# Performance work log

Hardware: AMD Instinct MI355X
Metric: run time of the kernel (lower is better)

## Reference

```python
import jax, jax.numpy as jnp
import numpy as np

TEMPERATURE = 0.5
B, D = 4096, 256


def setup_inputs() -> dict:
    key = jax.random.key(0)
    k1, k2 = jax.random.split(key)
    z_i = jax.random.normal(k1, (B, D), dtype=jnp.float32)
    z_j = jax.random.normal(k2, (B, D), dtype=jnp.float32)
    return {"z_i": z_i, "z_j": z_j}


def reference(z_i, z_j):
    batch = z_i.shape[0]
    n = 2 * batch
    z = jnp.concatenate([z_i, z_j], axis=0)                      # [2B, D]
    z = z / jnp.linalg.norm(z, axis=1, keepdims=True)            # L2-normalize rows
    # cosine_similarity of unit vectors == dot product -> single GEMM
    sim = jnp.einsum('id,jd->ij', z, z) / TEMPERATURE            # [2B, 2B]
    mask = jnp.eye(n, dtype=bool)
    sim = jnp.where(mask, -jnp.inf, sim)                         # mask self-similarity
    positives = jnp.concatenate(
        [jnp.diagonal(sim, offset=batch), jnp.diagonal(sim, offset=-batch)], axis=0
    )                                                            # [2B]
    loss = -positives + jax.nn.logsumexp(sim, axis=1)            # [2B]
    return loss.mean()
```

## Files before the change

kernel.cpp:

```cpp
#include <hip/hip_runtime.h>
#include <hip/hip_bf16.h>
#include <stdint.h>
#include <stddef.h>


#define B_ROWS 4096
#define D_DIM  256
#define N_ROWS 8192
#define BM 128
#define BN 128

typedef __bf16 bf16;
typedef bf16  bf16x8  __attribute__((ext_vector_type(8)));
typedef bf16  bf16x4  __attribute__((ext_vector_type(4)));
typedef float floatx4 __attribute__((ext_vector_type(4)));

__global__ __launch_bounds__(256) void normalize_kernel(
    const float* __restrict__ z_i, const float* __restrict__ z_j,
    bf16* __restrict__ zn, float* __restrict__ sumexp) {
  const int wave = threadIdx.x >> 6;
  const int lane = threadIdx.x & 63;
  const int row  = blockIdx.x * 4 + wave;
  const float* src = (row < B_ROWS) ? (z_i + (size_t)row * D_DIM)
                                    : (z_j + (size_t)(row - B_ROWS) * D_DIM);
  float4 v = ((const float4*)src)[lane];
  float ss = v.x * v.x + v.y * v.y + v.z * v.z + v.w * v.w;
  #pragma unroll
  for (int m = 1; m < 64; m <<= 1) ss += __shfl_xor(ss, m);
  const float rn = rsqrtf(ss) * 1.6986436f;
  bf16x4 o;
  o[0] = (bf16)(v.x * rn);
  o[1] = (bf16)(v.y * rn);
  o[2] = (bf16)(v.z * rn);
  o[3] = (bf16)(v.w * rn);
  ((bf16x4*)(zn + (size_t)row * D_DIM))[lane] = o;
  if (lane == 0) sumexp[row] = 0.f;
}

__global__ __launch_bounds__(512, 2) void simexp_kernel(
    const bf16* __restrict__ zn, float* __restrict__ sumexp,
    float* __restrict__ pos) {
  __shared__ __align__(16) bf16 Bs[2][BN * D_DIM];

  const int tid   = threadIdx.x;
  const int wave  = tid >> 6;
  const int lane  = tid & 63;
  const int lcol  = lane & 15;
  const int lquad = lane >> 4;
  const int wr = (wave >> 1) * 32;
  const int wc = (wave & 1) * 64;
  const int ri = blockIdx.x >> 2;
  const int cj = blockIdx.x & 3;
  const int row_base = ri * BM;
  const bool has_tail = (ri < 32 && cj >= 2);

  auto ct_of = [&](int t) { return (ri + 8 * cj + t) & 63; };

  auto stageB = [&](int buf, const bf16* src, int it0, int it1) {
    for (int it = it0; it < it1; ++it) {
      const int s   = it * 512 + tid;
      const int n   = s >> 5;
      const int kcs = s & 31;
      const int kc  = (kcs & 24) | ((kcs & 7) ^ (n & 7));
      __builtin_amdgcn_global_load_lds(
          (const __attribute__((address_space(1))) unsigned int*)
              (src + (size_t)n * D_DIM + kc * 8),
          (__attribute__((address_space(3))) unsigned int*)&Bs[buf][s * 8],
          16, 0, 0);
    }
  };

  stageB(0, zn + (size_t)row_base * D_DIM, 0, 8);
  stageB(1, zn + (size_t)ct_of(0) * BM * D_DIM, 0, 8);
  __syncthreads();

  floatx4 af[2][8];
  #pragma unroll
  for (int ti = 0; ti < 2; ++ti) {
    const int n = wr + ti * 16 + lcol;
    #pragma unroll
    for (int kq = 0; kq < 8; ++kq) {
      const int kc  = kq * 4 + lquad;
      const int kcs = (kc & 24) | ((kc & 7) ^ (n & 7));
      af[ti][kq] = *(const floatx4*)(&Bs[0][(n * 32 + kcs) * 8]);
    }
  }
  __syncthreads();

  float rowsum[2][4];
  #pragma unroll
  for (int ti = 0; ti < 2; ++ti)
    #pragma unroll
    for (int r = 0; r < 4; ++r) rowsum[ti][r] = 0.f;

#define MFMA_(A, B_, C) __builtin_amdgcn_mfma_f32_16x16x32_bf16( \
    __builtin_bit_cast(bf16x8, A), B_, C, 0, 0, 0)

#define QPHASE(ACC, Q)                                                    \
  {                                                                       \
    bf16x8 bfr[8];                                                        \
    const int n = wc + (Q) * 16 + lcol;                                   \
    _Pragma("unroll")                                                     \
    for (int kq = 0; kq < 8; ++kq) {                                      \
      const int kc  = kq * 4 + lquad;                                     \
      const int kcs = (kc & 24) | ((kc & 7) ^ (n & 7));                   \
      bfr[kq] = *(const bf16x8*)(bbase + n * D_DIM + kcs * 8);            \
    }                                                                     \
    ACC[0] = floatx4{0.f, 0.f, 0.f, 0.f};                                 \
    ACC[1] = floatx4{0.f, 0.f, 0.f, 0.f};                                 \
    _Pragma("unroll")                                                     \
    for (int kq = 0; kq < 8; ++kq) {                                      \
      ACC[0] = MFMA_(af[0][kq], bfr[kq], ACC[0]);                         \
      ACC[1] = MFMA_(af[1][kq], bfr[kq], ACC[1]);                         \
    }                                                                     \
  }

#define SLICE(ACC, Q, CB, DG)                                             \
  {                                                                       \
    float cs = 0.f;                                                       \
    _Pragma("unroll")                                                     \
    for (int ti = 0; ti < 2; ++ti) {                                      \
      _Pragma("unroll")                                                   \
      for (int r = 0; r < 4; ++r) {                                       \
        const float v = ACC[ti][r];                                       \
        float e = __builtin_amdgcn_exp2f(v);                              \
        if (DG) {                                                         \
          const int rg = row_base + wr + ti * 16 + lquad * 4 + r;         \
          const int cg = (CB) + wc + (Q) * 16 + lcol;                     \
          if (cg == rg) e = 0.f;                \
        }                                                                 \
        rowsum[ti][r] += e;                                               \
        cs += e;                                                          \
      }                                                                   \
    }                                                                     \
    cs += __shfl_xor(cs, 16);                                             \
    cs += __shfl_xor(cs, 32);                                             \
    if (!(DG) && lquad == 0)                                              \
      atomicAdd(&sumexp[(CB) + wc + (Q) * 16 + lcol], cs);                \
  }

  floatx4 a3[2];
  int  pcol3  = 0;
  bool pdiag3 = false;

  #pragma unroll 1
  for (int t = 0; t < 8; ++t) {
    const bf16* bbase = &Bs[(t + 1) & 1][0];
    const int sb = t & 1;
    if (t < 7) {
      stageB(sb, zn + (size_t)ct_of(t + 1) * BM * D_DIM, 0, 8);
    } else if (has_tail) {
      stageB(sb, zn + (size_t)((ri + 32) * BM + (cj - 2) * 64) * D_DIM, 0, 4);
    }
    const int  colb = ct_of(t) * BM;
    const bool diag = (cj == 0 && t == 0);

    floatx4 a0[2], a1[2], a2[2];
    QPHASE(a0, 0)
    if (t > 0) SLICE(a3, 3, pcol3, pdiag3)
    QPHASE(a1, 1)
    SLICE(a0, 0, colb, diag)
    QPHASE(a2, 2)
    SLICE(a1, 1, colb, diag)
    QPHASE(a3, 3)
    SLICE(a2, 2, colb, diag)
    pcol3 = colb;
    pdiag3 = diag;
    __syncthreads();
  }
  SLICE(a3, 3, pcol3, pdiag3)

  if (has_tail && wc == 0) {
    const int colb = (ri + 32) * BM + (cj - 2) * 64;
    const bf16* bbase = &Bs[1][0];
    floatx4 ta[2];
    #pragma unroll
    for (int Q = 0; Q < 4; ++Q) {
      QPHASE(ta, Q)
      float cs = 0.f;
      #pragma unroll
      for (int ti = 0; ti < 2; ++ti) {
        #pragma unroll
        for (int r = 0; r < 4; ++r) {
          const float v = ta[ti][r];
          const float e = __builtin_amdgcn_exp2f(v);
          const int rg = row_base + wr + ti * 16 + lquad * 4 + r;
          const int cg = colb + Q * 16 + lcol;
          if (cg == rg + B_ROWS) {
            const float p = v * 0.6931471805599453f;
            pos[rg] = p;
            pos[cg] = p;
          }
          rowsum[ti][r] += e;
          cs += e;
        }
      }
      cs += __shfl_xor(cs, 16);
      cs += __shfl_xor(cs, 32);
      if (lquad == 0) atomicAdd(&sumexp[colb + Q * 16 + lcol], cs);
    }
  }
#undef SLICE
#undef QPHASE
#undef MFMA_

  #pragma unroll
  for (int ti = 0; ti < 2; ++ti) {
    #pragma unroll
    for (int r = 0; r < 4; ++r) {
      float s2 = rowsum[ti][r];
      s2 += __shfl_xor(s2, 1);
      s2 += __shfl_xor(s2, 2);
      s2 += __shfl_xor(s2, 4);
      s2 += __shfl_xor(s2, 8);
      if (lcol == 0) {
        const int grow = row_base + wr + ti * 16 + lquad * 4 + r;
        atomicAdd(&sumexp[grow], s2);
      }
    }
  }
}

__global__ __launch_bounds__(1024) void reduce_kernel(
    const float* __restrict__ sumexp, const float* __restrict__ pos,
    float* __restrict__ out) {
  __shared__ float ws[16];
  const int tid = threadIdx.x;
  float s = 0.f;
  const float ln2 = 0.6931471805599453f;
  for (int k = tid; k < N_ROWS; k += 1024)
    s += __builtin_amdgcn_logf(sumexp[k]) * ln2 - pos[k];
  #pragma unroll
  for (int m = 1; m < 64; m <<= 1) s += __shfl_xor(s, m);
  const int wave = tid >> 6, lane = tid & 63;
  if (lane == 0) ws[wave] = s;
  __syncthreads();
  if (wave == 0) {
    float t = (lane < 16) ? ws[lane] : 0.f;
    #pragma unroll
    for (int m = 1; m < 16; m <<= 1) t += __shfl_xor(t, m);
    if (lane == 0) out[0] = t * (1.0f / N_ROWS);
  }
}

extern "C" void kernel_launch(void* const* d_in, const int* in_sizes, int n_in,
                              void* d_out, int out_size, void* d_ws,
                              size_t ws_size, hipStream_t stream) {
  const float* z_i = (const float*)d_in[0];
  const float* z_j = (const float*)d_in[1];
  float* out = (float*)d_out;

  bf16* zn = (bf16*)d_ws;
  float* sumexp = (float*)((char*)d_ws + (size_t)N_ROWS * D_DIM * sizeof(bf16));
  float* pos = sumexp + N_ROWS;

  normalize_kernel<<<N_ROWS / 4, 256, 0, stream>>>(z_i, z_j, zn, sumexp);
  simexp_kernel<<<256, 512, 0, stream>>>(zn, sumexp, pos);
  reduce_kernel<<<1, 1024, 0, stream>>>(sumexp, pos, out);
}
```

Baseline: 92.08 us.

## Stage B tiles in K-halves with finer pipelining and LDS column-sum accumulation

Splits each B tile into two K-halves held in a 4-slot LDS ring. Loads of the next tile's halves overlap MFMA on the current halves, synchronised with explicit vmcnt waits and raw s_barrier instead of full __syncthreads. Column-sum partials now go to LDS atomics and are flushed to global once per block, which cuts global atomic traffic. MFMA sections also get s_setprio boosts. The cost is more LDS (two extra buffers' worth plus a colsum array) and fragile hand-tuned waitcnt logic.

```diff
diff --git a/kernel.cpp b/kernel.cpp
--- a/kernel.cpp
+++ b/kernel.cpp
@@ -8,7 +8,6 @@
 #define D_DIM  256
 #define N_ROWS 8192
 #define BM 128
-#define BN 128
 
 typedef __bf16 bf16;
 typedef bf16  bf16x8  __attribute__((ext_vector_type(8)));
@@ -40,7 +39,8 @@
 __global__ __launch_bounds__(512, 2) void simexp_kernel(
     const bf16* __restrict__ zn, float* __restrict__ sumexp,
     float* __restrict__ pos) {
-  __shared__ __align__(16) bf16 Bs[2][BN * D_DIM];
+  __shared__ __align__(16) bf16 Hs[4][128 * 128];
+  __shared__ float colsum_s[9 * 128];
 
   const int tid   = threadIdx.x;
   const int wave  = tid >> 6;
@@ -56,8 +56,23 @@
 
   auto ct_of = [&](int t) { return (ri + 8 * cj + t) & 63; };
 
-  auto stageB = [&](int buf, const bf16* src, int it0, int it1) {
-    for (int it = it0; it < it1; ++it) {
+  auto stage_half = [&](int buf, const bf16* src, int kh) {
+    #pragma unroll
+    for (int it = 0; it < 4; ++it) {
+      const int s   = it * 512 + tid;
+      const int n   = s >> 4;
+      const int lcs = s & 15;
+      const int lc  = (lcs & 8) | ((lcs & 7) ^ (n & 7));
+      __builtin_amdgcn_global_load_lds(
+          (const __attribute__((address_space(1))) unsigned int*)
+              (src + (size_t)n * D_DIM + kh * 128 + lc * 8),
+          (__attribute__((address_space(3))) unsigned int*)&Hs[buf][s * 8],
+          16, 0, 0);
+    }
+  };
+  auto stage_tail = [&](int buf, const bf16* src) {
+    #pragma unroll
+    for (int it = 0; it < 4; ++it) {
       const int s   = it * 512 + tid;
       const int n   = s >> 5;
       const int kcs = s & 31;
@@ -65,14 +80,22 @@
       __builtin_amdgcn_global_load_lds(
           (const __attribute__((address_space(1))) unsigned int*)
               (src + (size_t)n * D_DIM + kc * 8),
-          (__attribute__((address_space(3))) unsigned int*)&Bs[buf][s * 8],
+          (__attribute__((address_space(3))) unsigned int*)&Hs[buf][s * 8],
           16, 0, 0);
     }
   };
 
-  stageB(0, zn + (size_t)row_base * D_DIM, 0, 8);
-  stageB(1, zn + (size_t)ct_of(0) * BM * D_DIM, 0, 8);
-  __syncthreads();
+  const bf16* Abase  = zn + (size_t)row_base * D_DIM;
+  const bf16* B0base = zn + (size_t)ct_of(0) * BM * D_DIM;
+  stage_half(0, Abase, 0);
+  stage_half(1, Abase, 1);
+  stage_half(2, B0base, 0);
+  stage_half(3, B0base, 1);
+  #pragma unroll 1
+  for (int s = tid; s < 9 * 128; s += 512) colsum_s[s] = 0.f;
+  asm volatile("s_waitcnt vmcnt(8)" ::: "memory");
+  __builtin_amdgcn_sched_barrier(0);
+  __builtin_amdgcn_s_barrier();
 
   floatx4 af[2][8];
   #pragma unroll
@@ -80,12 +103,15 @@
     const int n = wr + ti * 16 + lcol;
     #pragma unroll
     for (int kq = 0; kq < 8; ++kq) {
-      const int kc  = kq * 4 + lquad;
-      const int kcs = (kc & 24) | ((kc & 7) ^ (n & 7));
-      af[ti][kq] = *(const floatx4*)(&Bs[0][(n * 32 + kcs) * 8]);
-    }
-  }
-  __syncthreads();
+      const int kql = kq & 3;
+      const int lc  = kql * 4 + lquad;
+      const int lcs = (lc & 8) | ((lc & 7) ^ (n & 7));
+      af[ti][kq] = *(const floatx4*)(&Hs[kq >> 2][n * 128 + lcs * 8]);
+    }
+  }
+  asm volatile("s_waitcnt lgkmcnt(0)" ::: "memory");
+  __builtin_amdgcn_sched_barrier(0);
+  __builtin_amdgcn_s_barrier();
 
   float rowsum[2][4];
   #pragma unroll
@@ -96,26 +122,35 @@
 #define MFMA_(A, B_, C) __builtin_amdgcn_mfma_f32_16x16x32_bf16( \
     __builtin_bit_cast(bf16x8, A), B_, C, 0, 0, 0)
 
-#define QPHASE(ACC, Q)                                                    \
+#define QPHASE(ACC, Q, KH, BB)                                            \
   {                                                                       \
-    bf16x8 bfr[8];                                                        \
     const int n = wc + (Q) * 16 + lcol;                                   \
-    _Pragma("unroll")                                                     \
-    for (int kq = 0; kq < 8; ++kq) {                                      \
-      const int kc  = kq * 4 + lquad;                                     \
-      const int kcs = (kc & 24) | ((kc & 7) ^ (n & 7));                   \
-      bfr[kq] = *(const bf16x8*)(bbase + n * D_DIM + kcs * 8);            \
-    }                                                                     \
-    ACC[0] = floatx4{0.f, 0.f, 0.f, 0.f};                                 \
-    ACC[1] = floatx4{0.f, 0.f, 0.f, 0.f};                                 \
-    _Pragma("unroll")                                                     \
-    for (int kq = 0; kq < 8; ++kq) {                                      \
-      ACC[0] = MFMA_(af[0][kq], bfr[kq], ACC[0]);                         \
-      ACC[1] = MFMA_(af[1][kq], bfr[kq], ACC[1]);                         \
-    }                                                                     \
-  }
-
-#define SLICE(ACC, Q, CB, DG)                                             \
+    bf16x8 b0, b1, b2, b3;                                                \
+    { const int lc = 0 * 4 + lquad;                                       \
+      b0 = *(const bf16x8*)((BB) + n * 128 +                              \
+           (((lc & 8) | ((lc & 7) ^ (n & 7))) * 8)); }                    \
+    { const int lc = 1 * 4 + lquad;                                       \
+      b1 = *(const bf16x8*)((BB) + n * 128 +                              \
+           (((lc & 8) | ((lc & 7) ^ (n & 7))) * 8)); }                    \
+    { const int lc = 2 * 4 + lquad;                                       \
+      b2 = *(const bf16x8*)((BB) + n * 128 +                              \
+           (((lc & 8) | ((lc & 7) ^ (n & 7))) * 8)); }                    \
+    { const int lc = 3 * 4 + lquad;                                       \
+      b3 = *(const bf16x8*)((BB) + n * 128 +                              \
+           (((lc & 8) | ((lc & 7) ^ (n & 7))) * 8)); }                    \
+    __builtin_amdgcn_s_setprio(1);                                        \
+    ACC[0] = MFMA_(af[0][(KH)*4 + 0], b0, ACC[0]);                        \
+    ACC[1] = MFMA_(af[1][(KH)*4 + 0], b0, ACC[1]);                        \
+    ACC[0] = MFMA_(af[0][(KH)*4 + 1], b1, ACC[0]);                        \
+    ACC[1] = MFMA_(af[1][(KH)*4 + 1], b1, ACC[1]);                        \
+    ACC[0] = MFMA_(af[0][(KH)*4 + 2], b2, ACC[0]);                        \
+    ACC[1] = MFMA_(af[1][(KH)*4 + 2], b2, ACC[1]);                        \
+    ACC[0] = MFMA_(af[0][(KH)*4 + 3], b3, ACC[0]);                        \
+    ACC[1] = MFMA_(af[1][(KH)*4 + 3], b3, ACC[1]);                        \
+    __builtin_amdgcn_s_setprio(0);                                        \
+  }
+
+#define SLICE(ACC, Q, SLOT, COLB, DG)                                     \
   {                                                                       \
     float cs = 0.f;                                                       \
     _Pragma("unroll")                                                     \
@@ -126,8 +161,8 @@
         float e = __builtin_amdgcn_exp2f(v);                              \
         if (DG) {                                                         \
           const int rg = row_base + wr + ti * 16 + lquad * 4 + r;         \
-          const int cg = (CB) + wc + (Q) * 16 + lcol;                     \
-          if (cg == rg) e = 0.f;                \
+          const int cg = (COLB) + wc + (Q) * 16 + lcol;                   \
+          if (cg == rg) e = 0.f;                                          \
         }                                                                 \
         rowsum[ti][r] += e;                                               \
         cs += e;                                                          \
@@ -136,73 +171,139 @@
     cs += __shfl_xor(cs, 16);                                             \
     cs += __shfl_xor(cs, 32);                                             \
     if (!(DG) && lquad == 0)                                              \
-      atomicAdd(&sumexp[(CB) + wc + (Q) * 16 + lcol], cs);                \
-  }
-
-  floatx4 a3[2];
-  int  pcol3  = 0;
+      atomicAdd(&colsum_s[(SLOT) + wc + (Q) * 16 + lcol], cs);            \
+  }
+
+  floatx4 acc0[2], acc1[2], acc2[2], acc3[2];
+  floatx4 car[2];
+  int  pslot3 = 0, pcolb3 = 0;
   bool pdiag3 = false;
 
   #pragma unroll 1
   for (int t = 0; t < 8; ++t) {
-    const bf16* bbase = &Bs[(t + 1) & 1][0];
-    const int sb = t & 1;
-    if (t < 7) {
-      stageB(sb, zn + (size_t)ct_of(t + 1) * BM * D_DIM, 0, 8);
-    } else if (has_tail) {
-      stageB(sb, zn + (size_t)((ri + 32) * BM + (cj - 2) * 64) * D_DIM, 0, 4);
-    }
     const int  colb = ct_of(t) * BM;
     const bool diag = (cj == 0 && t == 0);
 
-    floatx4 a0[2], a1[2], a2[2];
-    QPHASE(a0, 0)
-    if (t > 0) SLICE(a3, 3, pcol3, pdiag3)
-    QPHASE(a1, 1)
-    SLICE(a0, 0, colb, diag)
-    QPHASE(a2, 2)
-    SLICE(a1, 1, colb, diag)
-    QPHASE(a3, 3)
-    SLICE(a2, 2, colb, diag)
-    pcol3 = colb;
-    pdiag3 = diag;
-    __syncthreads();
-  }
-  SLICE(a3, 3, pcol3, pdiag3)
-
-  if (has_tail && wc == 0) {
-    const int colb = (ri + 32) * BM + (cj - 2) * 64;
-    const bf16* bbase = &Bs[1][0];
-    floatx4 ta[2];
-    #pragma unroll
-    for (int Q = 0; Q < 4; ++Q) {
-      QPHASE(ta, Q)
-      float cs = 0.f;
+    {
+      const int h = 2 * t;
+      if (t < 7) {
+        stage_half(h & 3, zn + (size_t)ct_of(t + 1) * BM * D_DIM, 0);
+        asm volatile("s_waitcnt vmcnt(8)" ::: "memory");
+      } else if (has_tail) {
+        stage_tail(h & 3,
+                   zn + (size_t)((ri + 32) * BM + (cj - 2) * 64) * D_DIM);
+        asm volatile("s_waitcnt vmcnt(8)" ::: "memory");
+      } else {
+        asm volatile("s_waitcnt vmcnt(4)" ::: "memory");
+      }
+      __builtin_amdgcn_sched_barrier(0);
+      __builtin_amdgcn_s_barrier();
+      const bf16* bb = &Hs[(h + 2) & 3][0];
       #pragma unroll
       for (int ti = 0; ti < 2; ++ti) {
+        acc0[ti] = floatx4{0.f, 0.f, 0.f, 0.f};
+        acc1[ti] = floatx4{0.f, 0.f, 0.f, 0.f};
+        acc2[ti] = floatx4{0.f, 0.f, 0.f, 0.f};
+        acc3[ti] = floatx4{0.f, 0.f, 0.f, 0.f};
+      }
+      QPHASE(acc0, 0, 0, bb)
+      QPHASE(acc1, 1, 0, bb)
+      QPHASE(acc2, 2, 0, bb)
+      QPHASE(acc3, 3, 0, bb)
+    }
+
+    {
+      const int h = 2 * t + 1;
+      if (t < 7) {
+        stage_half(h & 3, zn + (size_t)ct_of(t + 1) * BM * D_DIM, 1);
+        asm volatile("s_waitcnt vmcnt(8)" ::: "memory");
+      } else if (has_tail) {
+        asm volatile("s_waitcnt vmcnt(4)" ::: "memory");
+      } else {
+        asm volatile("s_waitcnt vmcnt(0)" ::: "memory");
+      }
+      __builtin_amdgcn_sched_barrier(0);
+      __builtin_amdgcn_s_barrier();
+      const bf16* bb = &Hs[(h + 2) & 3][0];
+      QPHASE(acc0, 0, 1, bb)
+      if (t > 0) SLICE(car, 3, pslot3, pcolb3, pdiag3)
+      QPHASE(acc1, 1, 1, bb)
+      SLICE(acc0, 0, t * 128, colb, diag)
+      QPHASE(acc2, 2, 1, bb)
+      SLICE(acc1, 1, t * 128, colb, diag)
+      QPHASE(acc3, 3, 1, bb)
+      SLICE(acc2, 2, t * 128, colb, diag)
+      car[0] = acc3[0];
+      car[1] = acc3[1];
+      pslot3 = t * 128;
+      pcolb3 = colb;
+      pdiag3 = diag;
+    }
+  }
+  SLICE(car, 3, pslot3, pcolb3, pdiag3)
+
+  if (has_tail) {
+    asm volatile("s_waitcnt vmcnt(0)" ::: "memory");
+    __builtin_amdgcn_sched_barrier(0);
+    __builtin_amdgcn_s_barrier();
+    if (wc == 0) {
+      const int colb = (ri + 32) * BM + (cj - 2) * 64;
+      const bf16* bb = &Hs[2][0];
+      #pragma unroll
+      for (int Q = 0; Q < 4; ++Q) {
+        const int n = Q * 16 + lcol;
+        floatx4 ta[2];
+        ta[0] = floatx4{0.f, 0.f, 0.f, 0.f};
+        ta[1] = floatx4{0.f, 0.f, 0.f, 0.f};
         #pragma unroll
-        for (int r = 0; r < 4; ++r) {
-          const float v = ta[ti][r];
-          const float e = __builtin_amdgcn_exp2f(v);
-          const int rg = row_base + wr + ti * 16 + lquad * 4 + r;
-          const int cg = colb + Q * 16 + lcol;
-          if (cg == rg + B_ROWS) {
-            const float p = v * 0.6931471805599453f;
-            pos[rg] = p;
-            pos[cg] = p;
+        for (int kq = 0; kq < 8; ++kq) {
+          const int kc  = kq * 4 + lquad;
+          const int kcs = (kc & 24) | ((kc & 7) ^ (n & 7));
+          const bf16x8 b = *(const bf16x8*)(bb + n * 256 + kcs * 8);
+          ta[0] = MFMA_(af[0][kq], b, ta[0]);
+          ta[1] = MFMA_(af[1][kq], b, ta[1]);
+        }
+        float cs = 0.f;
+        #pragma unroll
+        for (int ti = 0; ti < 2; ++ti) {
+          #pragma unroll
+          for (int r = 0; r < 4; ++r) {
+            const float v = ta[ti][r];
+            const float e = __builtin_amdgcn_exp2f(v);
+            const int rg = row_base + wr + ti * 16 + lquad * 4 + r;
+            const int cg = colb + Q * 16 + lcol;
+            if (cg == rg + B_ROWS) {
+              const float p = v * 0.6931471805599453f;
+              pos[rg] = p;
+              pos[cg] = p;
+            }
+            rowsum[ti][r] += e;
+            cs += e;
           }
-          rowsum[ti][r] += e;
-          cs += e;
         }
-      }
-      cs += __shfl_xor(cs, 16);
-      cs += __shfl_xor(cs, 32);
-      if (lquad == 0) atomicAdd(&sumexp[colb + Q * 16 + lcol], cs);
+        cs += __shfl_xor(cs, 16);
+        cs += __shfl_xor(cs, 32);
+        if (lquad == 0) atomicAdd(&colsum_s[8 * 128 + Q * 16 + lcol], cs);
+      }
     }
   }
 #undef SLICE
 #undef QPHASE
 #undef MFMA_
+
+  __syncthreads();
+
+  #pragma unroll 1
+  for (int s = tid; s < 9 * 128; s += 512) {
+    const int tile = s >> 7, col = s & 127;
+    const float v = colsum_s[s];
+    if (tile < 8) {
+      if (!(cj == 0 && tile == 0))
+        atomicAdd(&sumexp[ct_of(tile) * BM + col], v);
+    } else if (has_tail && col < 64) {
+      atomicAdd(&sumexp[(ri + 32) * BM + (cj - 2) * 64 + col], v);
+    }
+  }
 
   #pragma unroll
   for (int ti = 0; ti < 2; ++ti) {
```

Result: slower. 95.49 us (+3.7%).

## Reshape per-wave tile to 64x32 so each B fragment feeds four MFMAs

Applied to the files above, without the earlier changes.

Changes the 8-wave layout from 4x2 waves of 32x64 sub-tiles to 2x4 waves of 64x32 sub-tiles. Each wave now holds four A row-fragments in registers and loads half as many B fragments from LDS per tile, reusing each across four MFMAs. The software pipeline is restructured from four column phases to two, with a carried accumulator overlapping exp work of one phase with the next phase's MFMAs. The doubled A fragments and accumulators raise register pressure, and the launch bounds are relaxed to 1 min block with waves_per_eu(2) to give the compiler room.

```diff
diff --git a/kernel.cpp b/kernel.cpp
--- a/kernel.cpp
+++ b/kernel.cpp
@@ -8,7 +8,6 @@
 #define D_DIM  256
 #define N_ROWS 8192
 #define BM 128
-#define BN 128
 
 typedef __bf16 bf16;
 typedef bf16  bf16x8  __attribute__((ext_vector_type(8)));
@@ -37,18 +36,20 @@
   if (lane == 0) sumexp[row] = 0.f;
 }
 
-__global__ __launch_bounds__(512, 2) void simexp_kernel(
+__global__ __launch_bounds__(512, 1)
+__attribute__((amdgpu_waves_per_eu(2)))
+void simexp_kernel(
     const bf16* __restrict__ zn, float* __restrict__ sumexp,
     float* __restrict__ pos) {
-  __shared__ __align__(16) bf16 Bs[2][BN * D_DIM];
+  __shared__ __align__(16) bf16 Bs[2][BM * D_DIM];
 
   const int tid   = threadIdx.x;
   const int wave  = tid >> 6;
   const int lane  = tid & 63;
   const int lcol  = lane & 15;
   const int lquad = lane >> 4;
-  const int wr = (wave >> 1) * 32;
-  const int wc = (wave & 1) * 64;
+  const int wr = (wave >> 2) * 64;
+  const int wc = (wave & 3) * 32;
   const int ri = blockIdx.x >> 2;
   const int cj = blockIdx.x & 3;
   const int row_base = ri * BM;
@@ -74,9 +75,9 @@
   stageB(1, zn + (size_t)ct_of(0) * BM * D_DIM, 0, 8);
   __syncthreads();
 
-  floatx4 af[2][8];
-  #pragma unroll
-  for (int ti = 0; ti < 2; ++ti) {
+  floatx4 af[4][8];
+  #pragma unroll
+  for (int ti = 0; ti < 4; ++ti) {
     const int n = wr + ti * 16 + lcol;
     #pragma unroll
     for (int kq = 0; kq < 8; ++kq) {
@@ -87,46 +88,47 @@
   }
   __syncthreads();
 
-  float rowsum[2][4];
-  #pragma unroll
-  for (int ti = 0; ti < 2; ++ti)
+  float rowsum[4][4];
+  #pragma unroll
+  for (int ti = 0; ti < 4; ++ti)
     #pragma unroll
     for (int r = 0; r < 4; ++r) rowsum[ti][r] = 0.f;
 
 #define MFMA_(A, B_, C) __builtin_amdgcn_mfma_f32_16x16x32_bf16( \
     __builtin_bit_cast(bf16x8, A), B_, C, 0, 0, 0)
 
-#define QPHASE(ACC, Q)                                                    \
+#define PHASE_(ACC, NCOL, BB)                                             \
   {                                                                       \
+    const int n = (NCOL);                                                 \
     bf16x8 bfr[8];                                                        \
-    const int n = wc + (Q) * 16 + lcol;                                   \
     _Pragma("unroll")                                                     \
     for (int kq = 0; kq < 8; ++kq) {                                      \
       const int kc  = kq * 4 + lquad;                                     \
       const int kcs = (kc & 24) | ((kc & 7) ^ (n & 7));                   \
-      bfr[kq] = *(const bf16x8*)(bbase + n * D_DIM + kcs * 8);            \
+      bfr[kq] = *(const bf16x8*)((BB) + n * D_DIM + kcs * 8);             \
     }                                                                     \
-    ACC[0] = floatx4{0.f, 0.f, 0.f, 0.f};                                 \
-    ACC[1] = floatx4{0.f, 0.f, 0.f, 0.f};                                 \
+    _Pragma("unroll")                                                     \
+    for (int ti = 0; ti < 4; ++ti) ACC[ti] = floatx4{0.f, 0.f, 0.f, 0.f}; \
     _Pragma("unroll")                                                     \
     for (int kq = 0; kq < 8; ++kq) {                                      \
-      ACC[0] = MFMA_(af[0][kq], bfr[kq], ACC[0]);                         \
-      ACC[1] = MFMA_(af[1][kq], bfr[kq], ACC[1]);                         \
+      _Pragma("unroll")                                                   \
+      for (int ti = 0; ti < 4; ++ti)                                      \
+        ACC[ti] = MFMA_(af[ti][kq], bfr[kq], ACC[ti]);                    \
     }                                                                     \
   }
 
-#define SLICE(ACC, Q, CB, DG)                                             \
+#define SLICE(ACC, CGB, DG)                                               \
   {                                                                       \
     float cs = 0.f;                                                       \
     _Pragma("unroll")                                                     \
-    for (int ti = 0; ti < 2; ++ti) {                                      \
+    for (int ti = 0; ti < 4; ++ti) {                                      \
       _Pragma("unroll")                                                   \
       for (int r = 0; r < 4; ++r) {                                       \
         const float v = ACC[ti][r];                                       \
         float e = __builtin_amdgcn_exp2f(v);                              \
         if (DG) {                                                         \
           const int rg = row_base + wr + ti * 16 + lquad * 4 + r;         \
-          const int cg = (CB) + wc + (Q) * 16 + lcol;                     \
+          const int cg = (CGB) + lcol;                                    \
           if (cg == rg) e = 0.f;                \
         }                                                                 \
         rowsum[ti][r] += e;                                               \
@@ -135,13 +137,12 @@
     }                                                                     \
     cs += __shfl_xor(cs, 16);                                             \
     cs += __shfl_xor(cs, 32);                                             \
-    if (!(DG) && lquad == 0)                                              \
-      atomicAdd(&sumexp[(CB) + wc + (Q) * 16 + lcol], cs);                \
-  }
-
-  floatx4 a3[2];
-  int  pcol3  = 0;
-  bool pdiag3 = false;
+    if (!(DG) && lquad == 0) atomicAdd(&sumexp[(CGB) + lcol], cs);        \
+  }
+
+  floatx4 accA[4], accB[4], carry[4];
+  int  pcgb  = 0;
+  bool pdiag = false;
 
   #pragma unroll 1
   for (int t = 0; t < 8; ++t) {
@@ -155,37 +156,34 @@
     const int  colb = ct_of(t) * BM;
     const bool diag = (cj == 0 && t == 0);
 
-    floatx4 a0[2], a1[2], a2[2];
-    QPHASE(a0, 0)
-    if (t > 0) SLICE(a3, 3, pcol3, pdiag3)
-    QPHASE(a1, 1)
-    SLICE(a0, 0, colb, diag)
-    QPHASE(a2, 2)
-    SLICE(a1, 1, colb, diag)
-    QPHASE(a3, 3)
-    SLICE(a2, 2, colb, diag)
-    pcol3 = colb;
-    pdiag3 = diag;
+    PHASE_(accA, wc + lcol, bbase)
+    if (t > 0) SLICE(carry, pcgb, pdiag)
+    PHASE_(accB, wc + 16 + lcol, bbase)
+    SLICE(accA, colb + wc, diag)
+    #pragma unroll
+    for (int ti = 0; ti < 4; ++ti) carry[ti] = accB[ti];
+    pcgb  = colb + wc + 16;
+    pdiag = diag;
     __syncthreads();
   }
-  SLICE(a3, 3, pcol3, pdiag3)
-
-  if (has_tail && wc == 0) {
+  SLICE(carry, pcgb, pdiag)
+
+  if (has_tail && (wave & 3) < 2) {
     const int colb = (ri + 32) * BM + (cj - 2) * 64;
     const bf16* bbase = &Bs[1][0];
-    floatx4 ta[2];
-    #pragma unroll
-    for (int Q = 0; Q < 4; ++Q) {
-      QPHASE(ta, Q)
+    floatx4 ta[4];
+    #pragma unroll
+    for (int tj = 0; tj < 2; ++tj) {
+      PHASE_(ta, wc + tj * 16 + lcol, bbase)
       float cs = 0.f;
       #pragma unroll
-      for (int ti = 0; ti < 2; ++ti) {
+      for (int ti = 0; ti < 4; ++ti) {
         #pragma unroll
         for (int r = 0; r < 4; ++r) {
           const float v = ta[ti][r];
           const float e = __builtin_amdgcn_exp2f(v);
           const int rg = row_base + wr + ti * 16 + lquad * 4 + r;
-          const int cg = colb + Q * 16 + lcol;
+          const int cg = colb + wc + tj * 16 + lcol;
           if (cg == rg + B_ROWS) {
             const float p = v * 0.6931471805599453f;
             pos[rg] = p;
@@ -197,15 +195,15 @@
       }
       cs += __shfl_xor(cs, 16);
       cs += __shfl_xor(cs, 32);
-      if (lquad == 0) atomicAdd(&sumexp[colb + Q * 16 + lcol], cs);
+      if (lquad == 0) atomicAdd(&sumexp[colb + wc + tj * 16 + lcol], cs);
     }
   }
 #undef SLICE
-#undef QPHASE
+#undef PHASE_
 #undef MFMA_
 
   #pragma unroll
-  for (int ti = 0; ti < 2; ++ti) {
+  for (int ti = 0; ti < 4; ++ti) {
     #pragma unroll
     for (int r = 0; r < 4; ++r) {
       float s2 = rowsum[ti][r];
```

Measured after the change: 94.28 us. 1.02x slower.

## Fuse normalize, similarity-exp, and reduce into one cooperative kernel with grid syncs

Applied to the files above, without the earlier changes.

Merges the three kernels into a single cooperative launch of 256 blocks. Each block normalizes 32 rows, the grid synchronizes, the block runs the similarity/exp tile work, and after a second grid sync block 0 performs the final log-sum reduction. The aim is to remove two kernel launch gaps. In exchange it adds two grid-wide barriers and a cooperative-launch requirement, which needs all 256 blocks to be co-resident.

```diff
diff --git a/kernel.cpp b/kernel.cpp
--- a/kernel.cpp
+++ b/kernel.cpp
@@ -1,4 +1,5 @@
 #include <hip/hip_runtime.h>
+#include <hip/hip_cooperative_groups.h>
 #include <hip/hip_bf16.h>
 #include <stdint.h>
 #include <stddef.h>
@@ -10,41 +11,45 @@
 #define BM 128
 #define BN 128
 
+namespace cg = cooperative_groups;
+
 typedef __bf16 bf16;
 typedef bf16  bf16x8  __attribute__((ext_vector_type(8)));
 typedef bf16  bf16x4  __attribute__((ext_vector_type(4)));
 typedef float floatx4 __attribute__((ext_vector_type(4)));
 
-__global__ __launch_bounds__(256) void normalize_kernel(
+__global__ __launch_bounds__(512, 2) void ntxent_fused(
     const float* __restrict__ z_i, const float* __restrict__ z_j,
-    bf16* __restrict__ zn, float* __restrict__ sumexp) {
-  const int wave = threadIdx.x >> 6;
-  const int lane = threadIdx.x & 63;
-  const int row  = blockIdx.x * 4 + wave;
-  const float* src = (row < B_ROWS) ? (z_i + (size_t)row * D_DIM)
-                                    : (z_j + (size_t)(row - B_ROWS) * D_DIM);
-  float4 v = ((const float4*)src)[lane];
-  float ss = v.x * v.x + v.y * v.y + v.z * v.z + v.w * v.w;
-  #pragma unroll
-  for (int m = 1; m < 64; m <<= 1) ss += __shfl_xor(ss, m);
-  const float rn = rsqrtf(ss) * 1.6986436f;
-  bf16x4 o;
-  o[0] = (bf16)(v.x * rn);
-  o[1] = (bf16)(v.y * rn);
-  o[2] = (bf16)(v.z * rn);
-  o[3] = (bf16)(v.w * rn);
-  ((bf16x4*)(zn + (size_t)row * D_DIM))[lane] = o;
-  if (lane == 0) sumexp[row] = 0.f;
-}
-
-__global__ __launch_bounds__(512, 2) void simexp_kernel(
-    const bf16* __restrict__ zn, float* __restrict__ sumexp,
-    float* __restrict__ pos) {
+    bf16* __restrict__ zn, float* __restrict__ sumexp,
+    float* __restrict__ pos, float* __restrict__ out) {
   __shared__ __align__(16) bf16 Bs[2][BN * D_DIM];
 
   const int tid   = threadIdx.x;
   const int wave  = tid >> 6;
   const int lane  = tid & 63;
+
+  #pragma unroll
+  for (int rr = 0; rr < 4; ++rr) {
+    const int row = blockIdx.x * 32 + wave * 4 + rr;
+    const float* src = (row < B_ROWS)
+                           ? (z_i + (size_t)row * D_DIM)
+                           : (z_j + (size_t)(row - B_ROWS) * D_DIM);
+    float4 v = ((const float4*)src)[lane];
+    float ss = v.x * v.x + v.y * v.y + v.z * v.z + v.w * v.w;
+    #pragma unroll
+    for (int m = 1; m < 64; m <<= 1) ss += __shfl_xor(ss, m);
+    const float rn = rsqrtf(ss) * 1.6986436f;
+    bf16x4 o;
+    o[0] = (bf16)(v.x * rn);
+    o[1] = (bf16)(v.y * rn);
+    o[2] = (bf16)(v.z * rn);
+    o[3] = (bf16)(v.w * rn);
+    ((bf16x4*)(zn + (size_t)row * D_DIM))[lane] = o;
+    if (lane == 0) sumexp[row] = 0.f;
+  }
+
+  cg::this_grid().sync();
+
   const int lcol  = lane & 15;
   const int lquad = lane >> 4;
   const int wr = (wave >> 1) * 32;
@@ -219,27 +224,25 @@
       }
     }
   }
-}
-
-__global__ __launch_bounds__(1024) void reduce_kernel(
-    const float* __restrict__ sumexp, const float* __restrict__ pos,
-    float* __restrict__ out) {
-  __shared__ float ws[16];
-  const int tid = threadIdx.x;
-  float s = 0.f;
-  const float ln2 = 0.6931471805599453f;
-  for (int k = tid; k < N_ROWS; k += 1024)
-    s += __builtin_amdgcn_logf(sumexp[k]) * ln2 - pos[k];
-  #pragma unroll
-  for (int m = 1; m < 64; m <<= 1) s += __shfl_xor(s, m);
-  const int wave = tid >> 6, lane = tid & 63;
-  if (lane == 0) ws[wave] = s;
-  __syncthreads();
-  if (wave == 0) {
-    float t = (lane < 16) ? ws[lane] : 0.f;
-    #pragma unroll
-    for (int m = 1; m < 16; m <<= 1) t += __shfl_xor(t, m);
-    if (lane == 0) out[0] = t * (1.0f / N_ROWS);
+
+  cg::this_grid().sync();
+  if (blockIdx.x == 0) {
+    float* ws = (float*)&Bs[0][0];
+    const float ln2 = 0.6931471805599453f;
+    float s = 0.f;
+    #pragma unroll 1
+    for (int k = tid; k < N_ROWS; k += 512)
+      s += __builtin_amdgcn_logf(sumexp[k]) * ln2 - pos[k];
+    #pragma unroll
+    for (int m = 1; m < 64; m <<= 1) s += __shfl_xor(s, m);
+    if (lane == 0) ws[wave] = s;
+    __syncthreads();
+    if (wave == 0) {
+      float tt = (lane < 8) ? ws[lane] : 0.f;
+      #pragma unroll
+      for (int m = 1; m < 8; m <<= 1) tt += __shfl_xor(tt, m);
+      if (lane == 0) out[0] = tt * (1.0f / N_ROWS);
+    }
   }
 }
 
@@ -254,7 +257,8 @@
   float* sumexp = (float*)((char*)d_ws + (size_t)N_ROWS * D_DIM * sizeof(bf16));
   float* pos = sumexp + N_ROWS;
 
-  normalize_kernel<<<N_ROWS / 4, 256, 0, stream>>>(z_i, z_j, zn, sumexp);
-  simexp_kernel<<<256, 512, 0, stream>>>(zn, sumexp, pos);
-  reduce_kernel<<<1, 1024, 0, stream>>>(sumexp, pos, out);
+  void* args[] = {(void*)&z_i, (void*)&z_j, (void*)&zn,
+                  (void*)&sumexp, (void*)&pos, (void*)&out};
+  hipLaunchCooperativeKernel((void*)ntxent_fused, dim3(256), dim3(512),
+                             args, 0, stream);
 }
```

After: 156.1 us. 69.5% more time.
